# Kernel optimization log

Measured on AMD Instinct MI355X. Metric: run time of the kernel, lower is better.

Reference implementation:

```python
import jax, jax.numpy as jnp
import numpy as np

HEIGHT, WIDTH = 32, 32
NUM_HEADS = 16
FREQUENCY = 10000.0


def _get_thetas(dim, height, width, frequency):
    # dim = head_dim, must be even. Returns (height*width, dim).
    half = dim // 2
    ifreq = 1.0 / (frequency ** (jnp.arange(half, dtype=jnp.float32) / half))
    freqs_h = jnp.arange(height, dtype=jnp.float32)[:, None] * ifreq[None, :]  # (h, half)
    freqs_w = jnp.arange(width, dtype=jnp.float32)[:, None] * ifreq[None, :]   # (w, half)
    theta_h = jnp.broadcast_to(freqs_h[:, None, :], (height, width, half))
    theta_w = jnp.broadcast_to(freqs_w[None, :, :], (height, width, half))
    theta = jnp.concatenate([theta_h, theta_w], axis=-1)  # (h, w, dim)
    return theta.reshape(height * width, dim)


def _add_rope(t, cos, sin):
    # t: (b, h, n, d); cos/sin: (n, d) broadcast over batch and heads
    x1, x2 = jnp.split(t, 2, axis=-1)
    t_rot = jnp.concatenate([-x2, x1], axis=-1)
    return t * cos + t_rot * sin


def setup_inputs() -> dict:
    key = jax.random.key(0)
    k1, k2, k3 = jax.random.split(key, 3)
    b, n, c = 8, HEIGHT * WIDTH, 1024
    tensor = jax.random.normal(k1, (b, n, c), dtype=jnp.float32)
    w_qkv = jax.random.normal(k2, (3 * c, c), dtype=jnp.float32) * (c ** -0.5)
    w_proj = jax.random.normal(k3, (c, c), dtype=jnp.float32) * (c ** -0.5)
    return {"tensor": tensor, "w_qkv": w_qkv, "w_proj": w_proj}


def reference(tensor, w_qkv, w_proj):
    b, n, c = tensor.shape
    hd = c // NUM_HEADS
    # QKV projection, split per-head last dim into q,k,v (matches torch chunk on dim=-1)
    qkv = jnp.einsum('bnc,fc->bnf', tensor, w_qkv)            # (b, n, 3c)
    qkv = qkv.reshape(b, n, NUM_HEADS, 3 * hd).transpose(0, 2, 1, 3)  # (b, H, n, 3*hd)
    q, k, v = jnp.split(qkv, 3, axis=-1)                      # each (b, H, n, hd)
    # 2D RoPE on q, k
    theta = _get_thetas(hd, HEIGHT, WIDTH, FREQUENCY).astype(tensor.dtype)  # (n, hd)
    cos, sin = jnp.cos(theta), jnp.sin(theta)
    q = _add_rope(q, cos, sin)
    k = _add_rope(k, cos, sin)
    # scaled dot product attention
    scale = hd ** -0.5
    scores = jnp.einsum('bhqd,bhkd->bhqk', q, k) * scale
    attn = jax.nn.softmax(scores, axis=-1)
    o = jnp.einsum('bhqk,bhkd->bhqd', attn, v)
    o = o.transpose(0, 2, 1, 3).reshape(b, n, c)
    return jnp.einsum('bnc,oc->bno', o, w_proj)
```

## Files before the change

### kernel.cpp

```cpp
#include <hip/hip_runtime.h>

typedef __attribute__((ext_vector_type(8))) short short8v;
typedef __attribute__((ext_vector_type(4))) float floatx4;
typedef __attribute__((ext_vector_type(4))) unsigned short ushortx4;

__device__ __forceinline__ unsigned short f2bf(float f){
  unsigned int u = __float_as_uint(f);
  u += 0x7fffu + ((u >> 16) & 1u);
  return (unsigned short)(u >> 16);
}

__device__ __forceinline__ void gload_lds16(const void* g, void* l){
  __builtin_amdgcn_global_load_lds((const __attribute__((address_space(1))) void*)g,
                                   (__attribute__((address_space(3))) void*)l, 16, 0, 0);
}

__global__ __launch_bounds__(256) void cvt4(const floatx4* __restrict__ s,
                                            ushortx4* __restrict__ d, int n4){
  int i = blockIdx.x * 256 + threadIdx.x;
  if(i < n4){
    floatx4 v = s[i];
    ushortx4 o;
    #pragma unroll
    for(int j = 0; j < 4; ++j) o[j] = f2bf(v[j]);
    d[i] = o;
  }
}

__global__ __launch_bounds__(256) void cs_init(float2* __restrict__ cs){
  int i = blockIdx.x * 256 + threadIdx.x;
  int p = i >> 6, d = i & 63;
  int y = p >> 5, x = p & 31;
  int dd = d & 31;
  float ifr = powf(10000.0f, -(float)dd * (1.0f / 32.0f));
  float th = (float)(d < 32 ? y : x) * ifr;
  cs[i].x = cosf(th);
  cs[i].y = sinf(th);
}

template<int EPI, int BM>
__global__ __launch_bounds__(512, 2) void gemm8(
    const unsigned short* __restrict__ A,
    const unsigned short* __restrict__ B,
    int K, int N, int NXB,
    float* __restrict__ Cf,
    const float2* __restrict__ cs,
    unsigned short* __restrict__ qw,
    unsigned short* __restrict__ kw,
    unsigned short* __restrict__ vtw)
{
  constexpr int MF = BM / 32;
  constexpr int WR = BM / 2;
  constexpr int AKH = BM * 64;
  __shared__ char lds[(BM + 256) * 256];
  const int tid = threadIdx.x;
  const int w = tid >> 6, lane = tid & 63;
  const int g = lane >> 4, c0 = lane & 15;
  const int wm = w >> 2, wn = w & 3;
  const int NT = K >> 6;

  const int per = gridDim.x >> 3;
  const int wg = (blockIdx.x & 7) * per + (blockIdx.x >> 3);
  const int by = wg / NXB, bx = wg % NXB;
  const size_t m0 = (size_t)by * BM;
  const size_t n0 = (size_t)bx * 256;

  const int row0 = tid >> 2;
  const int xch = (tid & 3) ^ ((tid >> 3) & 3);
  const unsigned short* sA0 = A + (m0 + row0) * K + xch * 8;
  const unsigned short* sA1 = A + (m0 + row0 + 128) * K + xch * 8;
  const unsigned short* sB0 = B + (n0 + row0) * K + xch * 8;
  const unsigned short* sB1 = B + (n0 + row0 + 128) * K + xch * 8;
  char* const Ald = lds;
  char* const Bld = lds + 4 * AKH;
  const int wb = w * 1024;

  auto stA = [&](int t, int buf, int kh){
    char* d = Ald + buf * 2 * AKH + kh * AKH + wb;
    gload_lds16(sA0 + t * 64 + kh * 32, d);
    if constexpr (BM == 256) gload_lds16(sA1 + t * 64 + kh * 32, d + 8192);
  };
  auto stB = [&](int t, int buf, int kh){
    char* d = Bld + buf * 32768 + kh * 16384 + wb;
    gload_lds16(sB0 + t * 64 + kh * 32, d);
    gload_lds16(sB1 + t * 64 + kh * 32, d + 8192);
  };

  const int archy = (g ^ ((c0 >> 1) & 3)) << 4;
  auto rdA = [&](int buf, int kh, int mf) -> short8v {
    return *(const short8v*)(Ald + buf * 2 * AKH + kh * AKH +
                             (wm * WR + mf * 16 + c0) * 64 + archy);
  };
  auto rdB = [&](int buf, int kh, int nf) -> short8v {
    return *(const short8v*)(Bld + buf * 32768 + kh * 16384 +
                             (wn * 64 + nf * 16 + c0) * 64 + archy);
  };

  floatx4 acc[MF][4] = {};

#define BARX() do{ __builtin_amdgcn_s_barrier(); __builtin_amdgcn_sched_barrier(0); }while(0)
#define VMC() do{ if constexpr (BM == 256) asm volatile("s_waitcnt vmcnt(4)" ::: "memory"); \
                  else                     asm volatile("s_waitcnt vmcnt(3)" ::: "memory"); }while(0)

  auto tile4 = [&](int t, int buf){
    const int ob = buf ^ 1;
    const int tn1 = (t + 1 < NT) ? t + 1 : NT - 1;
    const int tn2 = (t + 2 < NT) ? t + 2 : NT - 1;
    if constexpr (BM == 256){
      short8v am[4], bn[4];
      #pragma unroll
      for(int nf = 0; nf < 4; ++nf) bn[nf] = rdB(buf, 0, nf);
      #pragma unroll
      for(int mf = 0; mf < 4; ++mf) am[mf] = rdA(buf, 0, mf);
      stA(tn1, ob, 1); stB(tn1, ob, 1);
      BARX();
      __builtin_amdgcn_s_setprio(1);
      #pragma unroll
      for(int mf = 0; mf < 4; ++mf)
        #pragma unroll
        for(int nf = 0; nf < 4; ++nf)
          acc[mf][nf] = __builtin_amdgcn_mfma_f32_16x16x32_bf16(am[mf], bn[nf], acc[mf][nf], 0, 0, 0);
      __builtin_amdgcn_s_setprio(0);
      BARX();
      #pragma unroll
      for(int mf = 0; mf < 4; ++mf) am[mf] = rdA(buf, 0, 4 + mf);
      BARX();
      __builtin_amdgcn_s_setprio(1);
      #pragma unroll
      for(int mf = 0; mf < 4; ++mf)
        #pragma unroll
        for(int nf = 0; nf < 4; ++nf)
          acc[4 + mf][nf] = __builtin_amdgcn_mfma_f32_16x16x32_bf16(am[mf], bn[nf], acc[4 + mf][nf], 0, 0, 0);
      __builtin_amdgcn_s_setprio(0);
      BARX();
      #pragma unroll
      for(int nf = 0; nf < 4; ++nf) bn[nf] = rdB(buf, 1, nf);
      #pragma unroll
      for(int mf = 0; mf < 4; ++mf) am[mf] = rdA(buf, 1, mf);
      stA(tn2, buf, 0);
      BARX();
      __builtin_amdgcn_s_setprio(1);
      #pragma unroll
      for(int mf = 0; mf < 4; ++mf)
        #pragma unroll
        for(int nf = 0; nf < 4; ++nf)
          acc[mf][nf] = __builtin_amdgcn_mfma_f32_16x16x32_bf16(am[mf], bn[nf], acc[mf][nf], 0, 0, 0);
      __builtin_amdgcn_s_setprio(0);
      BARX();
      #pragma unroll
      for(int mf = 0; mf < 4; ++mf) am[mf] = rdA(buf, 1, 4 + mf);
      stB(tn2, buf, 0);
      BARX();
      __builtin_amdgcn_s_setprio(1);
      #pragma unroll
      for(int mf = 0; mf < 4; ++mf)
        #pragma unroll
        for(int nf = 0; nf < 4; ++nf)
          acc[4 + mf][nf] = __builtin_amdgcn_mfma_f32_16x16x32_bf16(am[mf], bn[nf], acc[4 + mf][nf], 0, 0, 0);
      __builtin_amdgcn_s_setprio(0);
      VMC();
      BARX();
    } else {
      short8v am[4], bn[4];
      #pragma unroll
      for(int nf = 0; nf < 4; ++nf) bn[nf] = rdB(buf, 0, nf);
      #pragma unroll
      for(int mf = 0; mf < 4; ++mf) am[mf] = rdA(buf, 0, mf);
      stA(tn1, ob, 1); stB(tn1, ob, 1);
      BARX();
      __builtin_amdgcn_s_setprio(1);
      #pragma unroll
      for(int mf = 0; mf < 4; ++mf)
        #pragma unroll
        for(int nf = 0; nf < 4; ++nf)
          acc[mf][nf] = __builtin_amdgcn_mfma_f32_16x16x32_bf16(am[mf], bn[nf], acc[mf][nf], 0, 0, 0);
      __builtin_amdgcn_s_setprio(0);
      BARX();
      #pragma unroll
      for(int nf = 0; nf < 4; ++nf) bn[nf] = rdB(buf, 1, nf);
      #pragma unroll
      for(int mf = 0; mf < 4; ++mf) am[mf] = rdA(buf, 1, mf);
      stA(tn2, buf, 0); stB(tn2, buf, 0);
      BARX();
      __builtin_amdgcn_s_setprio(1);
      #pragma unroll
      for(int mf = 0; mf < 4; ++mf)
        #pragma unroll
        for(int nf = 0; nf < 4; ++nf)
          acc[mf][nf] = __builtin_amdgcn_mfma_f32_16x16x32_bf16(am[mf], bn[nf], acc[mf][nf], 0, 0, 0);
      __builtin_amdgcn_s_setprio(0);
      VMC();
      BARX();
    }
  };

  stA(0, 0, 0); stB(0, 0, 0);
  stA(0, 0, 1); stB(0, 0, 1);
  stA(1, 1, 0); stB(1, 1, 0);
  VMC();
  BARX();

  for(int t = 0; t < NT; t += 2){ tile4(t, 0); tile4(t + 1, 1); }
  __syncthreads();
#undef BARX
#undef VMC

  if(EPI == 0){
    #pragma unroll
    for(int mf = 0; mf < MF; ++mf){
      size_t mrow = m0 + wm * WR + mf * 16 + g * 4;
      #pragma unroll
      for(int nf = 0; nf < 4; ++nf){
        size_t n = n0 + wn * 64 + nf * 16 + c0;
        #pragma unroll
        for(int r = 0; r < 4; ++r)
          Cf[(mrow + r) * N + n] = acc[mf][nf][r];
      }
    }
  } else {
    int t = (int)(n0 >> 6) + wn;
    int sect = t % 3, hh = t / 3;
    if(sect == 2){
      #pragma unroll
      for(int mf = 0; mf < MF; ++mf){
        size_t m = m0 + wm * WR + mf * 16 + g * 4;
        int b = (int)(m >> 10); int p = (int)(m & 1023);
        #pragma unroll
        for(int nf = 0; nf < 4; ++nf){
          int d = nf * 16 + c0;
          ushortx4 pk;
          #pragma unroll
          for(int r = 0; r < 4; ++r) pk[r] = f2bf(acc[mf][nf][r]);
          *(ushortx4*)(vtw + ((size_t)(b * 16 + hh) * 64 + d) * 1024 + p) = pk;
        }
      }
    } else {
      unsigned short* dst = (sect == 0) ? qw : kw;
      const float qs = (sect == 0) ? 0.18033688011112042f : 1.0f;
      #pragma unroll
      for(int mf = 0; mf < MF; ++mf){
        #pragma unroll
        for(int r = 0; r < 4; ++r){
          size_t m = m0 + wm * WR + mf * 16 + g * 4 + r;
          int b = (int)(m >> 10); int p = (int)(m & 1023);
          const float2* csr = cs + (size_t)p * 64;
          unsigned short* orow = dst + ((size_t)(b * 16 + hh) * 1024 + p) * 64;
          #pragma unroll
          for(int nf = 0; nf < 2; ++nf){
            int d = nf * 16 + c0;
            float x1 = acc[mf][nf][r], x2 = acc[mf][nf + 2][r];
            float2 cc1 = csr[d], cc2 = csr[d + 32];
            orow[d]      = f2bf((x1 * cc1.x - x2 * cc1.y) * qs);
            orow[d + 32] = f2bf((x2 * cc2.x + x1 * cc2.y) * qs);
          }
        }
      }
    }
  }
}

__global__ __launch_bounds__(512, 4) void attn_kernel(
    const unsigned short* __restrict__ qw,
    const unsigned short* __restrict__ kw,
    const unsigned short* __restrict__ vtw,
    unsigned short* __restrict__ ow)
{
  __shared__ char smem[65536];
  const int tid = threadIdx.x;
  const int w = tid >> 6, lane = tid & 63;
  const int g = lane >> 4, c0 = lane & 15;
  const int bb = blockIdx.x;
  const int xcd = bb & 7, slot = bb >> 3;
  const int bh = xcd + ((slot >> 2) << 3);
  const int qt = slot & 3;
  const size_t bhoff = (size_t)bh * 1024 * 64;
  const unsigned short* Qb = qw + bhoff;
  const unsigned short* Kb = kw + bhoff;
  const unsigned short* Vb = vtw + bhoff;
  const int q0 = qt * 256 + w * 32;
  char* Pw = smem + 32768 + w * 4096;

  const int srow = tid >> 3;
  const int sjx = ((tid & 7) ^ (srow & 7)) << 3;
  const unsigned short* ksrc = Kb + srow * 64 + sjx;
  const unsigned short* vsrc = Vb + (size_t)srow * 1024 + sjx;
  const int wbase = w * 1024;

  short8v bq[2][2];
  #pragma unroll
  for(int qf = 0; qf < 2; ++qf)
    #pragma unroll
    for(int i = 0; i < 2; ++i)
      bq[qf][i] = *(const short8v*)(Qb + (size_t)(q0 + qf * 16 + c0) * 64 + g * 8 + i * 32);

  floatx4 o[2][4] = {};
  float m_run[2] = {-1e30f, -1e30f};
  float l_part[2] = {0.0f, 0.0f};

  gload_lds16(ksrc, smem + wbase);
  gload_lds16(vsrc, smem + 8192 + wbase);
  __syncthreads();

  int cur = 0;
  for(int kv0 = 0; kv0 < 1024; kv0 += 64){
    char* Ksm = smem + cur * 16384;
    char* Vsm = smem + cur * 16384 + 8192;
    if(kv0 + 64 < 1024){
      char* alt = smem + (cur ^ 1) * 16384;
      gload_lds16(ksrc + (size_t)(kv0 + 64) * 64, alt + wbase);
      gload_lds16(vsrc + kv0 + 64, alt + 8192 + wbase);
    }
    floatx4 st[4][2];
    #pragma unroll
    for(int kf = 0; kf < 4; ++kf){
      const int krow = kf * 16 + c0;
      const char* kr = Ksm + (krow << 7);
      short8v ka0 = *(const short8v*)(kr + (((g    ) ^ (c0 & 7)) << 4));
      short8v ka1 = *(const short8v*)(kr + (((g + 4) ^ (c0 & 7)) << 4));
      #pragma unroll
      for(int qf = 0; qf < 2; ++qf){
        floatx4 z = {};
        z = __builtin_amdgcn_mfma_f32_16x16x32_bf16(ka0, bq[qf][0], z, 0, 0, 0);
        st[kf][qf] = __builtin_amdgcn_mfma_f32_16x16x32_bf16(ka1, bq[qf][1], z, 0, 0, 0);
      }
    }
    float vmax[2];
    #pragma unroll
    for(int qf = 0; qf < 2; ++qf){
      float vm = -1e30f;
      #pragma unroll
      for(int kf = 0; kf < 4; ++kf)
        #pragma unroll
        for(int r = 0; r < 4; ++r) vm = fmaxf(vm, st[kf][qf][r]);
      vm = fmaxf(vm, __shfl_xor(vm, 16));
      vm = fmaxf(vm, __shfl_xor(vm, 32));
      vmax[qf] = vm;
    }
    if(!__all(vmax[0] <= m_run[0] + 8.0f && vmax[1] <= m_run[1] + 8.0f)){
      #pragma unroll
      for(int qf = 0; qf < 2; ++qf){
        float m_new = fmaxf(m_run[qf], vmax[qf]);
        float sc = __builtin_amdgcn_exp2f(m_run[qf] - m_new);
        l_part[qf] *= sc;
        m_run[qf] = m_new;
        float f0 = __shfl(sc, g * 4 + 0);
        float f1 = __shfl(sc, g * 4 + 1);
        float f2 = __shfl(sc, g * 4 + 2);
        float f3 = __shfl(sc, g * 4 + 3);
        #pragma unroll
        for(int nf = 0; nf < 4; ++nf){
          o[qf][nf][0] *= f0; o[qf][nf][1] *= f1; o[qf][nf][2] *= f2; o[qf][nf][3] *= f3;
        }
      }
    }
    #pragma unroll
    for(int qf = 0; qf < 2; ++qf){
      float ps = 0.0f;
      #pragma unroll
      for(int kf = 0; kf < 4; ++kf){
        ushortx4 pk;
        #pragma unroll
        for(int r = 0; r < 4; ++r){
          float e = __builtin_amdgcn_exp2f(st[kf][qf][r] - m_run[qf]);
          ps += e;
          pk[r] = f2bf(e);
        }
        int byo = (qf << 11) + (c0 << 7) + (kf << 5) + (g << 3);
        byo ^= (c0 & 7) << 4;
        *(ushortx4*)(Pw + byo) = pk;
      }
      l_part[qf] += ps;
    }
    short8v pa[2][2];
    #pragma unroll
    for(int mf = 0; mf < 2; ++mf)
      #pragma unroll
      for(int i = 0; i < 2; ++i){
        int byo = (mf << 11) + (c0 << 7) + (i << 6) + (g << 4);
        byo ^= (c0 & 7) << 4;
        pa[mf][i] = *(const short8v*)(Pw + byo);
      }
    #pragma unroll
    for(int nf = 0; nf < 4; ++nf){
      const int vrow = nf * 16 + c0;
      const char* vr = Vsm + (vrow << 7);
      short8v v0 = *(const short8v*)(vr + (((g    ) ^ (c0 & 7)) << 4));
      short8v v1 = *(const short8v*)(vr + (((g + 4) ^ (c0 & 7)) << 4));
      #pragma unroll
      for(int mf = 0; mf < 2; ++mf){
        o[mf][nf] = __builtin_amdgcn_mfma_f32_16x16x32_bf16(pa[mf][0], v0, o[mf][nf], 0, 0, 0);
        o[mf][nf] = __builtin_amdgcn_mfma_f32_16x16x32_bf16(pa[mf][1], v1, o[mf][nf], 0, 0, 0);
      }
    }
    __syncthreads();
    cur ^= 1;
  }

  const int b = bh >> 4, hh = bh & 15;
  #pragma unroll
  for(int mf = 0; mf < 2; ++mf){
    l_part[mf] += __shfl_xor(l_part[mf], 16);
    l_part[mf] += __shfl_xor(l_part[mf], 32);
    float i0 = 1.0f / __shfl(l_part[mf], g * 4 + 0);
    float i1 = 1.0f / __shfl(l_part[mf], g * 4 + 1);
    float i2 = 1.0f / __shfl(l_part[mf], g * 4 + 2);
    float i3 = 1.0f / __shfl(l_part[mf], g * 4 + 3);
    #pragma unroll
    for(int nf = 0; nf < 4; ++nf){
      o[mf][nf][0] *= i0; o[mf][nf][1] *= i1; o[mf][nf][2] *= i2; o[mf][nf][3] *= i3;
      #pragma unroll
      for(int r = 0; r < 4; ++r){
        size_t row = (size_t)b * 1024 + q0 + mf * 16 + g * 4 + r;
        ow[row * 1024 + hh * 64 + nf * 16 + c0] = f2bf(o[mf][nf][r]);
      }
    }
  }
}


extern "C" void kernel_launch(void* const* d_in, const int* in_sizes, int n_in,
                              void* d_out, int out_size, void* d_ws, size_t ws_size,
                              hipStream_t stream){
  const float* tensor = (const float*)d_in[0];
  const float* w_qkv  = (const float*)d_in[1];
  const float* w_proj = (const float*)d_in[2];
  char* ws = (char*)d_ws;
  unsigned short* bfT  = (unsigned short*)(ws);
  unsigned short* bfWq = (unsigned short*)(ws + 16777216);
  unsigned short* bfWp = (unsigned short*)(ws + 23068672);
  float2*         cs   = (float2*)        (ws + 25165824);
  unsigned short* qw   = (unsigned short*)(ws + 25690112);
  unsigned short* kw   = (unsigned short*)(ws + 42467328);
  unsigned short* vtw  = (unsigned short*)(ws + 59244544);
  unsigned short* owp  = (unsigned short*)(ws + 76021760);

  cvt4<<<8192, 256, 0, stream>>>((const floatx4*)tensor, (ushortx4*)bfT, 2097152);
  cvt4<<<3072, 256, 0, stream>>>((const floatx4*)w_qkv,  (ushortx4*)bfWq, 786432);
  cvt4<<<1024, 256, 0, stream>>>((const floatx4*)w_proj, (ushortx4*)bfWp, 262144);
  cs_init<<<256, 256, 0, stream>>>(cs);

  gemm8<1, 128><<<768, 512, 0, stream>>>(bfT, bfWq, 1024, 3072, 12,
                                         nullptr, cs, qw, kw, vtw);
  attn_kernel<<<512, 512, 0, stream>>>(qw, kw, vtw, owp);
  gemm8<0, 128><<<256, 512, 0, stream>>>(owp, bfWp, 1024, 1024, 4,
                                         (float*)d_out, nullptr, nullptr, nullptr, nullptr);
}
```

Measured before the change: 163.9 us.

## Fuse prep kernels, simplify GEMM pipeline, pack RoPE output stores

Merges the three fp32-to-bf16 conversion launches and the cos/sin table init into a single prep kernel, cutting launch overhead. Removes the unused BM=256 GEMM path and changes the wait count to vmcnt(6) with an extra wait between the two k-halves. The RoPE epilogue now pairs adjacent lanes via shuffle so each writes a 32-bit word instead of two 16-bit stores. The changed vmcnt threshold alters how far prefetch runs ahead.

```diff
diff --git a/kernel.cpp b/kernel.cpp
--- a/kernel.cpp
+++ b/kernel.cpp
@@ -4,10 +4,10 @@
 typedef __attribute__((ext_vector_type(4))) float floatx4;
 typedef __attribute__((ext_vector_type(4))) unsigned short ushortx4;
 
-__device__ __forceinline__ unsigned short f2bf(float f){
+__device__ __forceinline__ unsigned int f2bf(float f){
   unsigned int u = __float_as_uint(f);
   u += 0x7fffu + ((u >> 16) & 1u);
-  return (unsigned short)(u >> 16);
+  return u >> 16;
 }
 
 __device__ __forceinline__ void gload_lds16(const void* g, void* l){
@@ -15,27 +15,33 @@
                                    (__attribute__((address_space(3))) void*)l, 16, 0, 0);
 }
 
-__global__ __launch_bounds__(256) void cvt4(const floatx4* __restrict__ s,
-                                            ushortx4* __restrict__ d, int n4){
+__global__ __launch_bounds__(256) void prep(
+    const floatx4* __restrict__ t,  ushortx4* __restrict__ dt,
+    const floatx4* __restrict__ wq, ushortx4* __restrict__ dq,
+    const floatx4* __restrict__ wp, ushortx4* __restrict__ dp,
+    float2* __restrict__ cs)
+{
   int i = blockIdx.x * 256 + threadIdx.x;
-  if(i < n4){
-    floatx4 v = s[i];
+  if(i < 3145728){
+    const floatx4* s; ushortx4* d; int j;
+    if(i < 2097152){ s = t;  d = dt; j = i; }
+    else if(i < 2883584){ s = wq; d = dq; j = i - 2097152; }
+    else { s = wp; d = dp; j = i - 2883584; }
+    floatx4 v = s[j];
     ushortx4 o;
     #pragma unroll
-    for(int j = 0; j < 4; ++j) o[j] = f2bf(v[j]);
-    d[i] = o;
+    for(int k = 0; k < 4; ++k) o[k] = (unsigned short)f2bf(v[k]);
+    d[j] = o;
+  } else {
+    int j = i - 3145728;
+    int p = j >> 6, dd = j & 63;
+    int y = p >> 5, x = p & 31;
+    int dm = dd & 31;
+    float ifr = powf(10000.0f, -(float)dm * (1.0f / 32.0f));
+    float th = (float)(dd < 32 ? y : x) * ifr;
+    cs[j].x = cosf(th);
+    cs[j].y = sinf(th);
   }
-}
-
-__global__ __launch_bounds__(256) void cs_init(float2* __restrict__ cs){
-  int i = blockIdx.x * 256 + threadIdx.x;
-  int p = i >> 6, d = i & 63;
-  int y = p >> 5, x = p & 31;
-  int dd = d & 31;
-  float ifr = powf(10000.0f, -(float)dd * (1.0f / 32.0f));
-  float th = (float)(d < 32 ? y : x) * ifr;
-  cs[i].x = cosf(th);
-  cs[i].y = sinf(th);
 }
 
 template<int EPI, int BM>
@@ -68,7 +74,6 @@
   const int row0 = tid >> 2;
   const int xch = (tid & 3) ^ ((tid >> 3) & 3);
   const unsigned short* sA0 = A + (m0 + row0) * K + xch * 8;
-  const unsigned short* sA1 = A + (m0 + row0 + 128) * K + xch * 8;
   const unsigned short* sB0 = B + (n0 + row0) * K + xch * 8;
   const unsigned short* sB1 = B + (n0 + row0 + 128) * K + xch * 8;
   char* const Ald = lds;
@@ -78,7 +83,6 @@
   auto stA = [&](int t, int buf, int kh){
     char* d = Ald + buf * 2 * AKH + kh * AKH + wb;
     gload_lds16(sA0 + t * 64 + kh * 32, d);
-    if constexpr (BM == 256) gload_lds16(sA1 + t * 64 + kh * 32, d + 8192);
   };
   auto stB = [&](int t, int buf, int kh){
     char* d = Bld + buf * 32768 + kh * 16384 + wb;
@@ -99,111 +103,55 @@
   floatx4 acc[MF][4] = {};
 
 #define BARX() do{ __builtin_amdgcn_s_barrier(); __builtin_amdgcn_sched_barrier(0); }while(0)
-#define VMC() do{ if constexpr (BM == 256) asm volatile("s_waitcnt vmcnt(4)" ::: "memory"); \
-                  else                     asm volatile("s_waitcnt vmcnt(3)" ::: "memory"); }while(0)
-
-  auto tile4 = [&](int t, int buf){
+#define VMC6() asm volatile("s_waitcnt vmcnt(6)" ::: "memory")
+
+  auto tile2 = [&](int t, int buf){
     const int ob = buf ^ 1;
     const int tn1 = (t + 1 < NT) ? t + 1 : NT - 1;
     const int tn2 = (t + 2 < NT) ? t + 2 : NT - 1;
-    if constexpr (BM == 256){
-      short8v am[4], bn[4];
-      #pragma unroll
-      for(int nf = 0; nf < 4; ++nf) bn[nf] = rdB(buf, 0, nf);
-      #pragma unroll
-      for(int mf = 0; mf < 4; ++mf) am[mf] = rdA(buf, 0, mf);
-      stA(tn1, ob, 1); stB(tn1, ob, 1);
-      BARX();
-      __builtin_amdgcn_s_setprio(1);
-      #pragma unroll
-      for(int mf = 0; mf < 4; ++mf)
-        #pragma unroll
-        for(int nf = 0; nf < 4; ++nf)
-          acc[mf][nf] = __builtin_amdgcn_mfma_f32_16x16x32_bf16(am[mf], bn[nf], acc[mf][nf], 0, 0, 0);
-      __builtin_amdgcn_s_setprio(0);
-      BARX();
-      #pragma unroll
-      for(int mf = 0; mf < 4; ++mf) am[mf] = rdA(buf, 0, 4 + mf);
-      BARX();
-      __builtin_amdgcn_s_setprio(1);
-      #pragma unroll
-      for(int mf = 0; mf < 4; ++mf)
-        #pragma unroll
-        for(int nf = 0; nf < 4; ++nf)
-          acc[4 + mf][nf] = __builtin_amdgcn_mfma_f32_16x16x32_bf16(am[mf], bn[nf], acc[4 + mf][nf], 0, 0, 0);
-      __builtin_amdgcn_s_setprio(0);
-      BARX();
-      #pragma unroll
-      for(int nf = 0; nf < 4; ++nf) bn[nf] = rdB(buf, 1, nf);
-      #pragma unroll
-      for(int mf = 0; mf < 4; ++mf) am[mf] = rdA(buf, 1, mf);
-      stA(tn2, buf, 0);
-      BARX();
-      __builtin_amdgcn_s_setprio(1);
-      #pragma unroll
-      for(int mf = 0; mf < 4; ++mf)
-        #pragma unroll
-        for(int nf = 0; nf < 4; ++nf)
-          acc[mf][nf] = __builtin_amdgcn_mfma_f32_16x16x32_bf16(am[mf], bn[nf], acc[mf][nf], 0, 0, 0);
-      __builtin_amdgcn_s_setprio(0);
-      BARX();
-      #pragma unroll
-      for(int mf = 0; mf < 4; ++mf) am[mf] = rdA(buf, 1, 4 + mf);
-      stB(tn2, buf, 0);
-      BARX();
-      __builtin_amdgcn_s_setprio(1);
-      #pragma unroll
-      for(int mf = 0; mf < 4; ++mf)
-        #pragma unroll
-        for(int nf = 0; nf < 4; ++nf)
-          acc[4 + mf][nf] = __builtin_amdgcn_mfma_f32_16x16x32_bf16(am[mf], bn[nf], acc[4 + mf][nf], 0, 0, 0);
-      __builtin_amdgcn_s_setprio(0);
-      VMC();
-      BARX();
-    } else {
-      short8v am[4], bn[4];
-      #pragma unroll
-      for(int nf = 0; nf < 4; ++nf) bn[nf] = rdB(buf, 0, nf);
-      #pragma unroll
-      for(int mf = 0; mf < 4; ++mf) am[mf] = rdA(buf, 0, mf);
-      stA(tn1, ob, 1); stB(tn1, ob, 1);
-      BARX();
-      __builtin_amdgcn_s_setprio(1);
-      #pragma unroll
-      for(int mf = 0; mf < 4; ++mf)
-        #pragma unroll
-        for(int nf = 0; nf < 4; ++nf)
-          acc[mf][nf] = __builtin_amdgcn_mfma_f32_16x16x32_bf16(am[mf], bn[nf], acc[mf][nf], 0, 0, 0);
-      __builtin_amdgcn_s_setprio(0);
-      BARX();
-      #pragma unroll
-      for(int nf = 0; nf < 4; ++nf) bn[nf] = rdB(buf, 1, nf);
-      #pragma unroll
-      for(int mf = 0; mf < 4; ++mf) am[mf] = rdA(buf, 1, mf);
-      stA(tn2, buf, 0); stB(tn2, buf, 0);
-      BARX();
-      __builtin_amdgcn_s_setprio(1);
-      #pragma unroll
-      for(int mf = 0; mf < 4; ++mf)
-        #pragma unroll
-        for(int nf = 0; nf < 4; ++nf)
-          acc[mf][nf] = __builtin_amdgcn_mfma_f32_16x16x32_bf16(am[mf], bn[nf], acc[mf][nf], 0, 0, 0);
-      __builtin_amdgcn_s_setprio(0);
-      VMC();
-      BARX();
-    }
+    short8v am[4], bn[4];
+    #pragma unroll
+    for(int nf = 0; nf < 4; ++nf) bn[nf] = rdB(buf, 0, nf);
+    #pragma unroll
+    for(int mf = 0; mf < 4; ++mf) am[mf] = rdA(buf, 0, mf);
+    stA(tn1, ob, 1); stB(tn1, ob, 1);
+    BARX();
+    __builtin_amdgcn_s_setprio(1);
+    #pragma unroll
+    for(int mf = 0; mf < 4; ++mf)
+      #pragma unroll
+      for(int nf = 0; nf < 4; ++nf)
+        acc[mf][nf] = __builtin_amdgcn_mfma_f32_16x16x32_bf16(am[mf], bn[nf], acc[mf][nf], 0, 0, 0);
+    __builtin_amdgcn_s_setprio(0);
+    VMC6();
+    BARX();
+    #pragma unroll
+    for(int nf = 0; nf < 4; ++nf) bn[nf] = rdB(buf, 1, nf);
+    #pragma unroll
+    for(int mf = 0; mf < 4; ++mf) am[mf] = rdA(buf, 1, mf);
+    stA(tn2, buf, 0); stB(tn2, buf, 0);
+    BARX();
+    __builtin_amdgcn_s_setprio(1);
+    #pragma unroll
+    for(int mf = 0; mf < 4; ++mf)
+      #pragma unroll
+      for(int nf = 0; nf < 4; ++nf)
+        acc[mf][nf] = __builtin_amdgcn_mfma_f32_16x16x32_bf16(am[mf], bn[nf], acc[mf][nf], 0, 0, 0);
+    __builtin_amdgcn_s_setprio(0);
+    VMC6();
+    BARX();
   };
 
   stA(0, 0, 0); stB(0, 0, 0);
   stA(0, 0, 1); stB(0, 0, 1);
   stA(1, 1, 0); stB(1, 1, 0);
-  VMC();
+  VMC6();
   BARX();
 
-  for(int t = 0; t < NT; t += 2){ tile4(t, 0); tile4(t + 1, 1); }
+  for(int t = 0; t < NT; t += 2){ tile2(t, 0); tile2(t + 1, 1); }
   __syncthreads();
 #undef BARX
-#undef VMC
+#undef VMC6
 
   if(EPI == 0){
     #pragma unroll
@@ -230,13 +178,14 @@
           int d = nf * 16 + c0;
           ushortx4 pk;
           #pragma unroll
-          for(int r = 0; r < 4; ++r) pk[r] = f2bf(acc[mf][nf][r]);
+          for(int r = 0; r < 4; ++r) pk[r] = (unsigned short)f2bf(acc[mf][nf][r]);
           *(ushortx4*)(vtw + ((size_t)(b * 16 + hh) * 64 + d) * 1024 + p) = pk;
         }
       }
     } else {
       unsigned short* dst = (sect == 0) ? qw : kw;
       const float qs = (sect == 0) ? 0.18033688011112042f : 1.0f;
+      const int codd = c0 & 1;
       #pragma unroll
       for(int mf = 0; mf < MF; ++mf){
         #pragma unroll
@@ -250,8 +199,13 @@
             int d = nf * 16 + c0;
             float x1 = acc[mf][nf][r], x2 = acc[mf][nf + 2][r];
             float2 cc1 = csr[d], cc2 = csr[d + 32];
-            orow[d]      = f2bf((x1 * cc1.x - x2 * cc1.y) * qs);
-            orow[d + 32] = f2bf((x2 * cc2.x + x1 * cc2.y) * qs);
+            unsigned int u1 = f2bf((x1 * cc1.x - x2 * cc1.y) * qs);
+            unsigned int u2 = f2bf((x2 * cc2.x + x1 * cc2.y) * qs);
+            unsigned int p1 = (unsigned int)__shfl_xor((int)u1, 1);
+            unsigned int p2 = (unsigned int)__shfl_xor((int)u2, 1);
+            unsigned int val = codd ? (p2 | (u2 << 16)) : (u1 | (p1 << 16));
+            int off = codd ? (d + 31) : d;
+            *(unsigned int*)(orow + off) = val;
           }
         }
       }
@@ -363,7 +317,7 @@
         for(int r = 0; r < 4; ++r){
           float e = __builtin_amdgcn_exp2f(st[kf][qf][r] - m_run[qf]);
           ps += e;
-          pk[r] = f2bf(e);
+          pk[r] = (unsigned short)f2bf(e);
         }
         int byo = (qf << 11) + (c0 << 7) + (kf << 5) + (g << 3);
         byo ^= (c0 & 7) << 4;
@@ -411,7 +365,7 @@
       #pragma unroll
       for(int r = 0; r < 4; ++r){
         size_t row = (size_t)b * 1024 + q0 + mf * 16 + g * 4 + r;
-        ow[row * 1024 + hh * 64 + nf * 16 + c0] = f2bf(o[mf][nf][r]);
+        ow[row * 1024 + hh * 64 + nf * 16 + c0] = (unsigned short)f2bf(o[mf][nf][r]);
       }
     }
   }
@@ -434,10 +388,9 @@
   unsigned short* vtw  = (unsigned short*)(ws + 59244544);
   unsigned short* owp  = (unsigned short*)(ws + 76021760);
 
-  cvt4<<<8192, 256, 0, stream>>>((const floatx4*)tensor, (ushortx4*)bfT, 2097152);
-  cvt4<<<3072, 256, 0, stream>>>((const floatx4*)w_qkv,  (ushortx4*)bfWq, 786432);
-  cvt4<<<1024, 256, 0, stream>>>((const floatx4*)w_proj, (ushortx4*)bfWp, 262144);
-  cs_init<<<256, 256, 0, stream>>>(cs);
+  prep<<<12544, 256, 0, stream>>>((const floatx4*)tensor, (ushortx4*)bfT,
+                                  (const floatx4*)w_qkv,  (ushortx4*)bfWq,
+                                  (const floatx4*)w_proj, (ushortx4*)bfWp, cs);
 
   gemm8<1, 128><<<768, 512, 0, stream>>>(bfT, bfWq, 1024, 3072, 12,
                                          nullptr, cs, qw, kw, vtw);
```

Result: no change. 160.9 us (-1.9%).
